# Kernel tuning notes

Hardware: AMD Instinct MI355X
Metric: run time of the kernel (lower is better)

Reference implementation:

```python
import jax, jax.numpy as jnp
import numpy as np

N0, N1, N2 = 60000, 15000, 3750
K, P = 32, 15
R0 = 0.5  # kernel extent at level 0; doubles per level (first_subsampling_dl*deform_radius scaled to unit-cube data)


def kpconv(q_pts, s_pts, neigh_idx, feats, kpoints, W, extent):
    """Rigid KPConv. q_pts [Nq,3], s_pts [Ns,3], neigh_idx [Nq,K] (shadow=Ns),
    feats [Ns,Cin], kpoints [P,3] unit-scale, W [P,Cin,Cout]."""
    s_pts_p = jnp.concatenate([s_pts, jnp.full((1, 3), 1e6, s_pts.dtype)], 0)
    feats_p = jnp.concatenate([feats, jnp.zeros((1, feats.shape[1]), feats.dtype)], 0)
    neigh_pts = s_pts_p[neigh_idx]                       # [Nq,K,3] gather
    neigh_f = feats_p[neigh_idx]                         # [Nq,K,Cin] gather
    diff = neigh_pts - q_pts[:, None, :]                 # [Nq,K,3]
    dist = jnp.sqrt(jnp.sum((diff[:, :, None, :] - kpoints[None, None] * extent) ** 2, -1))
    infl = jnp.maximum(0.0, 1.0 - dist / extent)         # [Nq,K,P] linear influence
    fk = jnp.einsum('nkp,nkc->npc', infl, neigh_f)       # per-kernel-point aggregation
    out = jnp.einsum('npc,pco->no', fk, W)
    return jax.nn.leaky_relu(out, 0.1)


def detection_scores(neighbor, features):
    # verbatim translation of KPFCNN.detection_scores (eval mode)
    n_total = features.shape[0]
    feats = jnp.concatenate([features, jnp.zeros_like(features[:1])], 0)
    neighbor = jnp.concatenate([neighbor, jnp.full_like(neighbor[:1], n_total)], 0)
    feats = feats / (jnp.max(feats) + 1e-6)
    nf = feats[neighbor]                                 # [N+1,K,C]
    nnum = jnp.maximum(jnp.sum(jnp.sum(nf, -1) != 0, -1, keepdims=True), 1)
    mean_f = jnp.sum(nf, 1) / nnum
    local_max_score = jax.nn.softplus(feats - mean_f)
    depth_max = jnp.max(feats, 1, keepdims=True)
    all_scores = local_max_score * (feats / (1e-6 + depth_max))
    scores = jnp.max(all_scores, 1, keepdims=True)
    detected = jnp.max((feats == jnp.max(nf, 1)).astype(feats.dtype), 1, keepdims=True)
    return (scores * detected)[:-1]


def reference(features, points0, points1, points2, neighbors0, neighbors1, neighbors2,
              pools0, pools1, upsamples0, upsamples1, kpoints, W1, W2, W3, W4, W5, Wu1, Wu2):
    # ---- encoder ----
    f = kpconv(points0, points0, neighbors0, features, kpoints, W1, R0)      # simple         [N0,64]
    skip0 = f
    f = kpconv(points1, points0, pools0, f, kpoints, W2, R0)                 # simple_strided [N1,64]
    f = kpconv(points1, points1, neighbors1, f, kpoints, W3, 2 * R0)         # simple         [N1,128]
    skip1 = f
    f = kpconv(points2, points1, pools1, f, kpoints, W4, 2 * R0)             # simple_strided [N2,128]
    f = kpconv(points2, points2, neighbors2, f, kpoints, W5, 4 * R0)         # simple         [N2,256]
    # ---- decoder: nearest_upsample + skip concat + unary ----
    f = jnp.concatenate([f[upsamples1[:, 0]], skip1], 1)                     # [N1,384] (1.5*256)
    f = jax.nn.leaky_relu(f @ Wu1, 0.1)                                      # unary          [N1,128]
    f = jnp.concatenate([f[upsamples0[:, 0]], skip0], 1)                     # [N0,192]
    f = f @ Wu2                                                              # last_unary     [N0,32]
    scores = detection_scores(neighbors0, f)
    fnorm = f / jnp.maximum(jnp.linalg.norm(f, axis=-1, keepdims=True), 1e-12)
    return fnorm, scores


def setup_inputs() -> dict:
    key = jax.random.key(0)
    ks = jax.random.split(key, 20)
    inp = {
        'features': jax.random.normal(ks[0], (N0, 1), jnp.float32),
        'points0': jax.random.uniform(ks[1], (N0, 3), jnp.float32),
        'points1': jax.random.uniform(ks[2], (N1, 3), jnp.float32),
        'points2': jax.random.uniform(ks[3], (N2, 3), jnp.float32),
        'neighbors0': jax.random.randint(ks[4], (N0, K), 0, N0, jnp.int32),
        'neighbors1': jax.random.randint(ks[5], (N1, K), 0, N1, jnp.int32),
        'neighbors2': jax.random.randint(ks[6], (N2, K), 0, N2, jnp.int32),
        'pools0': jax.random.randint(ks[7], (N1, K), 0, N0, jnp.int32),
        'pools1': jax.random.randint(ks[8], (N2, K), 0, N1, jnp.int32),
        'upsamples0': jax.random.randint(ks[9], (N0, 1), 0, N1, jnp.int32),
        'upsamples1': jax.random.randint(ks[10], (N1, 1), 0, N2, jnp.int32),
        'kpoints': jax.random.normal(ks[11], (P, 3), jnp.float32) * 0.5,
    }
    def w(k, shape, fan_in):
        return jax.random.normal(k, shape, jnp.float32) / np.sqrt(fan_in)
    inp['W1'] = w(ks[12], (P, 1, 64), P * 1)
    inp['W2'] = w(ks[13], (P, 64, 64), P * 64)
    inp['W3'] = w(ks[14], (P, 64, 128), P * 64)
    inp['W4'] = w(ks[15], (P, 128, 128), P * 128)
    inp['W5'] = w(ks[16], (P, 128, 256), P * 128)
    inp['Wu1'] = w(ks[17], (384, 128), 384)
    inp['Wu2'] = w(ks[18], (192, 32), 192)
    return inp
```

## Files before the change

### kernel.cpp

```cpp
#include <hip/hip_runtime.h>
#include <math.h>

static const int cN0 = 60000;
static const int cN1 = 15000;
static const int cN2 = 3750;

typedef __bf16 bf16x8 __attribute__((ext_vector_type(8)));
typedef float f32x4 __attribute__((ext_vector_type(4)));

#define GLOAD_LDS16(gsrc, ldst)                                                        \
  __builtin_amdgcn_global_load_lds((const __attribute__((address_space(1))) void*)(gsrc), \
                                   (__attribute__((address_space(3))) void*)(ldst), 16, 0, 0)

__global__ __launch_bounds__(256) void prep_kernel(
    const float* __restrict__ pts0, const float* __restrict__ feat,
    const float* __restrict__ pts1, const float* __restrict__ pts2,
    const float* __restrict__ W2, const float* __restrict__ W3, const float* __restrict__ W4,
    const float* __restrict__ W5, const float* __restrict__ Wu1, const float* __restrict__ Wu2,
    float4* __restrict__ pk0, float4* __restrict__ pk1, float4* __restrict__ pk2,
    __bf16* __restrict__ T2, __bf16* __restrict__ T3, __bf16* __restrict__ T4,
    __bf16* __restrict__ T5, __bf16* __restrict__ Tu1, __bf16* __restrict__ Tu2,
    unsigned* __restrict__ gm) {
  int role = blockIdx.y;
  int tid = blockIdx.x * 256 + threadIdx.x;
  int stride = gridDim.x * 256;
  if (role == 0 && tid == 0) gm[0] = 0u;
  if (role < 3) {
    const float* p = role == 0 ? pts0 : (role == 1 ? pts1 : pts2);
    float4* o = role == 0 ? pk0 : (role == 1 ? pk1 : pk2);
    int n = role == 0 ? cN0 : (role == 1 ? cN1 : cN2);
    for (int i = tid; i < n; i += stride) {
      float4 v;
      v.x = p[(size_t)i * 3 + 0];
      v.y = p[(size_t)i * 3 + 1];
      v.z = p[(size_t)i * 3 + 2];
      v.w = role == 0 ? feat[i] : 0.f;
      o[i] = v;
    }
  } else {
    const float* src;
    __bf16* dst;
    int Kd, Nd;
    switch (role) {
      case 3: src = W2;  dst = T2;  Kd = 960;  Nd = 64;  break;
      case 4: src = W3;  dst = T3;  Kd = 960;  Nd = 128; break;
      case 5: src = W4;  dst = T4;  Kd = 1920; Nd = 128; break;
      case 6: src = W5;  dst = T5;  Kd = 1920; Nd = 256; break;
      case 7: src = Wu1; dst = Tu1; Kd = 384;  Nd = 128; break;
      default: src = Wu2; dst = Tu2; Kd = 192; Nd = 32;  break;
    }
    int total = Kd * Nd;
    for (int e = tid; e < total; e += stride) {
      int n = e / Kd, k = e % Kd;
      dst[e] = (__bf16)src[(size_t)k * Nd + n];
    }
  }
}

__global__ __launch_bounds__(512) void kpconv_l1(
    const float4* __restrict__ pk, const int* __restrict__ neigh,
    const float* __restrict__ kpts, const float* __restrict__ W1,
    __bf16* __restrict__ f0, float extent) {
  const int t = threadIdx.x;
  const int n0b = blockIdx.x * 32;
  __shared__ float s_nb[32][32][4];
  __shared__ float s_fk[32][16];
  __shared__ float s_W[960];
  for (int i = t; i < 960; i += 512) s_W[i] = W1[i];
  #pragma unroll
  for (int i = 0; i < 2; ++i) {
    int e = t + i * 512;
    int pt = e & 31, k = e >> 5;
    int idx = neigh[(size_t)(n0b + pt) * 32 + k];
    *(float4*)&s_nb[k][pt][0] = pk[idx];
  }
  __syncthreads();
  const int lane = t & 63, wave = t >> 6;
  const int g = lane >> 4, p_raw = lane & 15;
  const int p = p_raw < 15 ? p_raw : 0;
  const int pt = wave * 4 + g;
  const int n = n0b + pt;
  const float inv = 1.f / extent;
  float4 q = pk[n];
  const float kx = q.x + kpts[p * 3 + 0] * extent;
  const float ky = q.y + kpts[p * 3 + 1] * extent;
  const float kz = q.z + kpts[p * 3 + 2] * extent;
  float fk = 0.f;
  #pragma unroll 8
  for (int k = 0; k < 32; ++k) {
    f32x4 rec = *(const f32x4*)&s_nb[k][pt][0];
    float dx = rec[0] - kx, dy = rec[1] - ky, dz = rec[2] - kz;
    float d = sqrtf(dx * dx + dy * dy + dz * dz);
    fk += fmaxf(0.f, 1.f - d * inv) * rec[3];
  }
  if (p_raw < 15) s_fk[pt][p_raw] = fk;
  __syncthreads();
  #pragma unroll
  for (int o = 0; o < 4; ++o) {
    int e = o * 512 + t;
    int opt = e >> 6, c = e & 63;
    float acc = 0.f;
    #pragma unroll
    for (int pp = 0; pp < 15; ++pp) acc += s_fk[opt][pp] * s_W[pp * 64 + c];
    acc = acc > 0.f ? acc : 0.1f * acc;
    f0[(size_t)(n0b + opt) * 64 + c] = (__bf16)acc;
  }
}

template <int CIN, int COUT, int BM, bool BDBUF>
__global__ __launch_bounds__(512) void kpconv_fused(
    const float4* __restrict__ qp, const float4* __restrict__ sp,
    const int* __restrict__ neigh, const __bf16* __restrict__ F,
    const float* __restrict__ kpts, const __bf16* __restrict__ BT,
    __bf16* __restrict__ out, int M, float extent) {
  constexpr int KK = 15 * CIN;
  constexpr int KT = KK / 64;
  constexpr int CPRow = CIN / 8;
  constexpr int G = CIN / 64;
  constexpr int GS = 64 / G;
  constexpr int NB = BM / 2;
  constexpr int CPW = CIN / 64;
  constexpr int FBUF = 64 * CIN;
  constexpr int RG = BM / 16;
  constexpr int CG = 8 / RG;
  constexpr int NJ = COUT / (16 * CG);
  constexpr int SMEM_FK = BM * KK * 2;
  constexpr int SMEM = SMEM_FK + 2 * 1280 + BM * 16 + 2 * FBUF * 2;

  __shared__ __align__(16) char smem[SMEM];
  __bf16* s_fk   = (__bf16*)smem;
  __bf16* s_infl = (__bf16*)(smem + SMEM_FK);
  float4* s_q    = (float4*)(smem + SMEM_FK + 2 * 1280);
  __bf16* s_F    = (__bf16*)(smem + SMEM_FK + 2 * 1280 + BM * 16);
  __bf16* s_B    = s_F;

  const int t = threadIdx.x;
  const int w = t >> 6, l = t & 63;
  const int c16 = l & 15, g4 = l >> 4;
  const int m0 = blockIdx.x * BM;
  const int* nb_base = neigh + (size_t)m0 * 32;
  int rlim = (M - m0) * 32 - 1;
  if (rlim > BM * 32 - 1) rlim = BM * 32 - 1;

  const int gb = t / CPRow;
  const int ch = t % CPRow;
  int idxg[NB][G];
  #pragma unroll
  for (int b = 0; b < NB; ++b)
    #pragma unroll
    for (int j = 0; j < G; ++j) {
      int r = b * 64 + gb + j * GS;
      idxg[b][j] = nb_base[r < rlim ? r : rlim];
    }
  const int row_i = (t >> 2) & 63;
  const int pq4 = (t & 3) * 4;
  const int pt_i = row_i >> 5, kk_i = row_i & 31;
  int idxi[NB];
  #pragma unroll
  for (int b = 0; b < NB; ++b) {
    int r = b * 64 + row_i;
    idxi[b] = nb_base[r < rlim ? r : rlim];
  }
  const float inv = 1.f / extent;
  float kpx[4], kpy[4], kpz[4];
  #pragma unroll
  for (int pi = 0; pi < 4; ++pi) {
    int p = pq4 + pi; if (p > 14) p = 14;
    kpx[pi] = kpts[p * 3 + 0] * extent;
    kpy[pi] = kpts[p * 3 + 1] * extent;
    kpz[pi] = kpts[p * 3 + 2] * extent;
  }
  if (t < BM) { int n = m0 + t; s_q[t] = qp[n < M ? n : M - 1]; }

  auto stageF = [&](int buf, const int (&ig)[G]) {
    #pragma unroll
    for (int j = 0; j < G; ++j) {
      int k = (gb + j * GS) & 31;
      const __bf16* src = F + (size_t)ig[j] * CIN + (ch ^ ((k >> 3) & 3)) * 8;
      GLOAD_LDS16(src, s_F + buf * FBUF + (j * 512 + t) * 8);
    }
  };
  auto inflC = [&](const float4& spv, int b, float (&v)[4]) {
    float4 q = s_q[b * 2 + pt_i];
    float sx = spv.x - q.x, sy = spv.y - q.y, sz = spv.z - q.z;
    #pragma unroll
    for (int pi = 0; pi < 4; ++pi) {
      float dx = sx - kpx[pi], dy = sy - kpy[pi], dz = sz - kpz[pi];
      float d = sqrtf(dx * dx + dy * dy + dz * dz);
      v[pi] = fmaxf(0.f, 1.f - d * inv);
    }
  };
  auto inflStore = [&](const float (&v)[4]) {
    if (t < 256) {
      #pragma unroll
      for (int pi = 0; pi < 4; ++pi) {
        int p = pq4 + pi;
        if (p < 15) s_infl[pt_i * 640 + p * 40 + kk_i] = (__bf16)v[pi];
      }
    }
  };
  auto mfmaBatch = [&](int b, int buf) {
    const int pt_loc = w / 4;
    const int cc0 = (w & 3) * CPW;
    const __bf16* Fb = s_F + buf * FBUF + pt_loc * (32 * CIN);
    bf16x8 a = *(const bf16x8*)&s_infl[pt_loc * 640 + c16 * 40 + g4 * 8];
    const int row = b * 2 + pt_loc;
    #pragma unroll
    for (int ci = 0; ci < CPW; ++ci) {
      const int cc = cc0 + ci;
      const int Lc = cc * 2 + (c16 >> 3);
      const int pc = Lc ^ g4;
      bf16x8 bv;
      #pragma unroll
      for (int j = 0; j < 8; ++j)
        bv[j] = Fb[(g4 * 8 + j) * CIN + pc * 8 + (c16 & 7)];
      f32x4 acc = __builtin_amdgcn_mfma_f32_16x16x32_bf16(a, bv, (f32x4){0.f, 0.f, 0.f, 0.f}, 0, 0, 0);
      #pragma unroll
      for (int r = 0; r < 4; ++r) {
        int p = g4 * 4 + r;
        if (p < 15) {
          int Lf = p * CPRow + Lc;
          int phys = (Lf & ~7) | ((Lf & 7) ^ (row & 7));
          s_fk[(size_t)row * KK + phys * 8 + (c16 & 7)] = (__bf16)acc[r];
        }
      }
    }
  };

  asm volatile("s_waitcnt lgkmcnt(0)" ::: "memory");
  __builtin_amdgcn_s_barrier();
  __builtin_amdgcn_sched_barrier(0);

  float4 spc, spn;
  {
    stageF(0, idxg[0]);
    float4 sp0 = sp[idxi[0]];
    spc = sp[idxi[1 < NB ? 1 : 0]];
    float v0[4];
    inflC(sp0, 0, v0);
    inflStore(v0);
  }
  __builtin_amdgcn_sched_barrier(0);
  #pragma unroll
  for (int b = 0; b < NB; ++b) {
    if (b + 1 < NB) stageF((b + 1) & 1, idxg[b + 1]);
    if (b + 2 < NB) spn = sp[idxi[b + 2]];
    float vn[4];
    if (b + 1 < NB) inflC(spc, b + 1, vn);
    if (b == NB - 1)      { asm volatile("s_waitcnt vmcnt(0)" ::: "memory"); }
    else if (b == NB - 2) { if (G == 1) asm volatile("s_waitcnt vmcnt(1)" ::: "memory");
                            else        asm volatile("s_waitcnt vmcnt(2)" ::: "memory"); }
    else                  { if (G == 1) asm volatile("s_waitcnt vmcnt(2)" ::: "memory");
                            else        asm volatile("s_waitcnt vmcnt(3)" ::: "memory"); }
    asm volatile("s_waitcnt lgkmcnt(0)" ::: "memory");
    __builtin_amdgcn_s_barrier();
    __builtin_amdgcn_sched_barrier(0);
    mfmaBatch(b, b & 1);
    asm volatile("s_waitcnt lgkmcnt(0)" ::: "memory");
    __builtin_amdgcn_s_barrier();
    __builtin_amdgcn_sched_barrier(0);
    if (b + 1 < NB) { inflStore(vn); spc = spn; }
  }
  __syncthreads();

  const int wr = w / CG, wc = w % CG;
  f32x4 acc[NJ];
  #pragma unroll
  for (int j = 0; j < NJ; ++j) acc[j] = (f32x4){0.f, 0.f, 0.f, 0.f};
  auto stageB = [&](int buf, int kt) {
    #pragma unroll
    for (int rnd = 0; rnd < COUT / 64; ++rnd) {
      int slot = rnd * 512 + t;
      int row = slot >> 3, bch = slot & 7;
      GLOAD_LDS16(BT + (size_t)row * KK + kt * 64 + (bch ^ (row & 7)) * 8,
                  s_B + buf * (COUT * 64) + slot * 8);
    }
  };
  const __bf16* fkrow = s_fk + (size_t)(wr * 16 + c16) * KK;
  auto computeTile = [&](int kt, int buf) {
    bf16x8 af[2];
    #pragma unroll
    for (int s = 0; s < 2; ++s)
      af[s] = *(const bf16x8*)&fkrow[(kt * 8 + ((s * 4 + g4) ^ (c16 & 7))) * 8];
    const __bf16* Bb = s_B + buf * (COUT * 64);
    #pragma unroll
    for (int j = 0; j < NJ; ++j) {
      int n = wc * (16 * NJ) + j * 16 + c16;
      #pragma unroll
      for (int s = 0; s < 2; ++s) {
        bf16x8 bf = *(const bf16x8*)&Bb[n * 64 + ((s * 4 + g4) ^ (n & 7)) * 8];
        acc[j] = __builtin_amdgcn_mfma_f32_16x16x32_bf16(af[s], bf, acc[j], 0, 0, 0);
      }
    }
  };
  if (BDBUF) {
    stageB(0, 0);
    __syncthreads();
    for (int kt = 0; kt < KT; ++kt) {
      if (kt + 1 < KT) stageB((kt + 1) & 1, kt + 1);
      computeTile(kt, kt & 1);
      __syncthreads();
    }
  } else {
    for (int kt = 0; kt < KT; ++kt) {
      stageB(0, kt);
      __syncthreads();
      computeTile(kt, 0);
      __syncthreads();
    }
  }
  #pragma unroll
  for (int j = 0; j < NJ; ++j)
    #pragma unroll
    for (int r = 0; r < 4; ++r) {
      int row = m0 + wr * 16 + g4 * 4 + r;
      int col = wc * (16 * NJ) + j * 16 + c16;
      if (row < M) {
        float v = acc[j][r];
        v = v > 0.f ? v : 0.1f * v;
        out[(size_t)row * COUT + col] = (__bf16)v;
      }
    }
}

template <bool LEAKY, bool GATHER>
__global__ __launch_bounds__(256, 2) void gemm_mfma(
    const __bf16* __restrict__ A1, const __bf16* __restrict__ A2,
    const int* __restrict__ gidx, const int K1,
    const __bf16* __restrict__ BT, __bf16* __restrict__ Cout,
    const int M, const int N, const int KK) {
  __shared__ __bf16 sA[2][4096];
  __shared__ __bf16 sB[2][4096];
  const int t = threadIdx.x;
  const int lane = t & 63, wave = t >> 6;
  const int wr = wave >> 1, wc = wave & 1;
  const int m0 = blockIdx.y * 64, n0 = blockIdx.x * 64;
  const int K2 = KK - K1;

  const __bf16* a1row[2];
  const __bf16* a2row[2];
  const __bf16* brow_[2];
  int csrc[2], wbase[2];
  #pragma unroll
  for (int r = 0; r < 2; ++r) {
    int slot = r * 256 + wave * 64 + lane;
    int row = slot >> 3;
    csrc[r] = ((slot & 7) ^ (row & 7)) * 8;
    wbase[r] = (r * 256 + wave * 64) * 8;
    int gm = m0 + row; if (gm > M - 1) gm = M - 1;
    if (GATHER) {
      a1row[r] = A1 + (size_t)gidx[gm] * K1;
      a2row[r] = A2 + (size_t)gm * (size_t)K2;
    } else {
      a1row[r] = A1 + (size_t)gm * (size_t)KK;
    }
    int gn = n0 + row; if (gn > N - 1) gn = N - 1;
    brow_[r] = BT + (size_t)gn * (size_t)KK;
  }

  int offA[2][2], offB[2][2];
  #pragma unroll
  for (int i = 0; i < 2; ++i)
    #pragma unroll
    for (int s = 0; s < 2; ++s) {
      int ra = wr * 32 + i * 16 + (lane & 15);
      int rb = wc * 32 + i * 16 + (lane & 15);
      int chn = s * 4 + (lane >> 4);
      offA[i][s] = ra * 64 + (chn ^ (ra & 7)) * 8;
      offB[i][s] = rb * 64 + (chn ^ (rb & 7)) * 8;
    }

  f32x4 acc[2][2];
  #pragma unroll
  for (int i = 0; i < 2; ++i)
    #pragma unroll
    for (int j = 0; j < 2; ++j) acc[i][j] = (f32x4){0.f, 0.f, 0.f, 0.f};

  auto stage = [&](int buf, int k0) {
    #pragma unroll
    for (int r = 0; r < 2; ++r) {
      int kg = k0 + csrc[r];
      const __bf16* asrc;
      if (GATHER) asrc = (kg < K1) ? (a1row[r] + kg) : (a2row[r] + (kg - K1));
      else        asrc = a1row[r] + kg;
      GLOAD_LDS16(asrc, &sA[buf][wbase[r]]);
      GLOAD_LDS16(brow_[r] + kg, &sB[buf][wbase[r]]);
    }
  };

  stage(0, 0);
  __syncthreads();
  const int nk = KK >> 6;
  int cur = 0;
  for (int kt = 0; kt < nk; ++kt) {
    if (kt + 1 < nk) stage(cur ^ 1, (kt + 1) << 6);
    #pragma unroll
    for (int s = 0; s < 2; ++s) {
      bf16x8 a0 = *(const bf16x8*)&sA[cur][offA[0][s]];
      bf16x8 a1 = *(const bf16x8*)&sA[cur][offA[1][s]];
      bf16x8 b0 = *(const bf16x8*)&sB[cur][offB[0][s]];
      bf16x8 b1 = *(const bf16x8*)&sB[cur][offB[1][s]];
      acc[0][0] = __builtin_amdgcn_mfma_f32_16x16x32_bf16(a0, b0, acc[0][0], 0, 0, 0);
      acc[0][1] = __builtin_amdgcn_mfma_f32_16x16x32_bf16(a0, b1, acc[0][1], 0, 0, 0);
      acc[1][0] = __builtin_amdgcn_mfma_f32_16x16x32_bf16(a1, b0, acc[1][0], 0, 0, 0);
      acc[1][1] = __builtin_amdgcn_mfma_f32_16x16x32_bf16(a1, b1, acc[1][1], 0, 0, 0);
    }
    __syncthreads();
    cur ^= 1;
  }

  #pragma unroll
  for (int i = 0; i < 2; ++i)
    #pragma unroll
    for (int j = 0; j < 2; ++j)
      #pragma unroll
      for (int g = 0; g < 4; ++g) {
        int row = m0 + wr * 32 + i * 16 + (lane >> 4) * 4 + g;
        int col = n0 + wc * 32 + j * 16 + (lane & 15);
        if (row < M && col < N) {
          float v = acc[i][j][g];
          if (LEAKY) v = v > 0.f ? v : 0.1f * v;
          Cout[(size_t)row * N + col] = (__bf16)v;
        }
      }
}

__global__ __launch_bounds__(256) void d2_kernel(
    const __bf16* __restrict__ f5b, const __bf16* __restrict__ f0b,
    const int* __restrict__ up0, const __bf16* __restrict__ BT,
    float* __restrict__ f6, int M, unsigned* __restrict__ gmax) {
  __shared__ __bf16 sA[128 * 192];
  __shared__ __bf16 sB[32 * 192];
  __shared__ int s_g[128];
  __shared__ float s_max[4];
  const int t = threadIdx.x;
  const int m0 = blockIdx.x * 128;
  if (t < 128) { int m = m0 + t; s_g[t] = up0[m < M ? m : M - 1]; }
  __syncthreads();
  #pragma unroll
  for (int rnd = 0; rnd < 3; ++rnd) {
    int slot = rnd * 256 + t;
    int row = slot / 24, chd = slot % 24;
    int chs = (chd & ~7) | ((chd & 7) ^ (row & 7));
    GLOAD_LDS16(BT + (size_t)row * 192 + chs * 8, sB + slot * 8);
  }
  #pragma unroll
  for (int rnd = 0; rnd < 12; ++rnd) {
    int slot = rnd * 256 + t;
    int row = slot / 24, chd = slot % 24;
    int chs = (chd & ~7) | ((chd & 7) ^ (row & 7));
    int m = m0 + row; if (m > M - 1) m = M - 1;
    const __bf16* src = (chs < 16) ? (f5b + (size_t)s_g[row] * 128 + chs * 8)
                                   : (f0b + (size_t)m * 64 + (chs - 16) * 8);
    GLOAD_LDS16(src, sA + slot * 8);
  }
  __syncthreads();
  const int w = t >> 6, lane = t & 63;
  const int c16 = lane & 15, g4 = lane >> 4;
  f32x4 acc[2][2];
  #pragma unroll
  for (int i = 0; i < 2; ++i)
    #pragma unroll
    for (int j = 0; j < 2; ++j) acc[i][j] = (f32x4){0.f, 0.f, 0.f, 0.f};
  #pragma unroll
  for (int ks = 0; ks < 6; ++ks) {
    bf16x8 a[2], b[2];
    #pragma unroll
    for (int i = 0; i < 2; ++i) {
      int row = w * 32 + i * 16 + c16;
      int chunk = ks * 4 + g4;
      int phys = (chunk & ~7) | ((chunk & 7) ^ (row & 7));
      a[i] = *(const bf16x8*)&sA[(row * 24 + phys) * 8];
    }
    #pragma unroll
    for (int j = 0; j < 2; ++j) {
      int n = j * 16 + c16;
      int chunk = ks * 4 + g4;
      int phys = (chunk & ~7) | ((chunk & 7) ^ (n & 7));
      b[j] = *(const bf16x8*)&sB[(n * 24 + phys) * 8];
    }
    #pragma unroll
    for (int i = 0; i < 2; ++i)
      #pragma unroll
      for (int j = 0; j < 2; ++j)
        acc[i][j] = __builtin_amdgcn_mfma_f32_16x16x32_bf16(a[i], b[j], acc[i][j], 0, 0, 0);
  }
  float lmax = 0.f;
  #pragma unroll
  for (int i = 0; i < 2; ++i)
    #pragma unroll
    for (int j = 0; j < 2; ++j)
      #pragma unroll
      for (int g = 0; g < 4; ++g) {
        int row = m0 + w * 32 + i * 16 + g4 * 4 + g;
        int col = j * 16 + c16;
        if (row < M) {
          float v = acc[i][j][g];
          lmax = fmaxf(lmax, v);
          f6[(size_t)row * 32 + col] = v;
        }
      }
  #pragma unroll
  for (int s = 32; s >= 1; s >>= 1) lmax = fmaxf(lmax, __shfl_xor(lmax, s, 64));
  if (lane == 0) s_max[w] = lmax;
  __syncthreads();
  if (t == 0) {
    float mm = fmaxf(fmaxf(s_max[0], s_max[1]), fmaxf(s_max[2], s_max[3]));
    atomicMax(gmax, __float_as_uint(mm));
  }
}

__global__ __launch_bounds__(512) void detect_kernel(
    const float* __restrict__ f6, const int* __restrict__ neigh,
    const float* __restrict__ gm_ptr, float* __restrict__ out_fnorm,
    float* __restrict__ out_scores, int N) {
  int n = blockIdx.x * 16 + (threadIdx.x >> 5);
  int c = threadIdx.x & 31;
  if (n >= N) return;
  float denom = gm_ptr[0] + 1e-6f;
  float fown = f6[(size_t)n * 32 + c];
  int idx_l = neigh[(size_t)n * 32 + c];
  float colsum = 0.f, colmax = -1e30f;
  for (int k = 0; k < 32; ++k) {
    int idx = __shfl(idx_l, k, 32);
    float v = f6[(size_t)idx * 32 + c];
    colsum += v;
    colmax = fmaxf(colmax, v);
  }
  float fs = fown / denom;
  float mean = (colsum / denom) * (1.f / 32.f);
  float x = fs - mean;
  float lms = fmaxf(x, 0.f) + log1pf(expf(-fabsf(x)));
  float dm = fs;
  #pragma unroll
  for (int s = 16; s >= 1; s >>= 1) dm = fmaxf(dm, __shfl_xor(dm, s, 32));
  float as = lms * fs / (1e-6f + dm);
  float sc = as;
  #pragma unroll
  for (int s = 16; s >= 1; s >>= 1) sc = fmaxf(sc, __shfl_xor(sc, s, 32));
  float det = (fown == colmax) ? 1.f : 0.f;
  #pragma unroll
  for (int s = 16; s >= 1; s >>= 1) det = fmaxf(det, __shfl_xor(det, s, 32));
  float nn2 = fown * fown;
  #pragma unroll
  for (int s = 16; s >= 1; s >>= 1) nn2 += __shfl_xor(nn2, s, 32);
  float inv_nrm = 1.f / fmaxf(sqrtf(nn2), 1e-12f);
  out_fnorm[(size_t)n * 32 + c] = fown * inv_nrm;
  if (c == 0) out_scores[n] = sc * det;
}

extern "C" void kernel_launch(void* const* d_in, const int* in_sizes, int n_in,
                              void* d_out, int out_size, void* d_ws, size_t ws_size,
                              hipStream_t stream) {
  const float* features  = (const float*)d_in[0];
  const float* points0   = (const float*)d_in[1];
  const float* points1   = (const float*)d_in[2];
  const float* points2   = (const float*)d_in[3];
  const int* neighbors0  = (const int*)d_in[4];
  const int* neighbors1  = (const int*)d_in[5];
  const int* neighbors2  = (const int*)d_in[6];
  const int* pools0      = (const int*)d_in[7];
  const int* pools1      = (const int*)d_in[8];
  const int* upsamples0  = (const int*)d_in[9];
  const int* upsamples1  = (const int*)d_in[10];
  const float* kpoints   = (const float*)d_in[11];
  const float* W1  = (const float*)d_in[12];
  const float* W2  = (const float*)d_in[13];
  const float* W3  = (const float*)d_in[14];
  const float* W4  = (const float*)d_in[15];
  const float* W5  = (const float*)d_in[16];
  const float* Wu1 = (const float*)d_in[17];
  const float* Wu2 = (const float*)d_in[18];

  const float R0 = 0.5f;

  char* wp = (char*)d_ws;
  auto alloc = [&](size_t bytes) {
    char* r = wp;
    wp += (bytes + 255) & ~(size_t)255;
    return r;
  };
  __bf16* f0b  = (__bf16*)alloc((size_t)cN0 * 64 * 2);
  __bf16* f1b  = (__bf16*)alloc((size_t)cN1 * 64 * 2);
  __bf16* f2b  = (__bf16*)alloc((size_t)cN1 * 128 * 2);
  __bf16* f3b  = (__bf16*)alloc((size_t)cN2 * 128 * 2);
  __bf16* f4b  = (__bf16*)alloc((size_t)cN2 * 256 * 2);
  __bf16* f5b  = (__bf16*)alloc((size_t)cN1 * 128 * 2);
  float*  f6   = (float*)alloc((size_t)cN0 * 32 * 4);
  __bf16* WT2  = (__bf16*)alloc(960 * 64 * 2);
  __bf16* WT3  = (__bf16*)alloc(960 * 128 * 2);
  __bf16* WT4  = (__bf16*)alloc(1920 * 128 * 2);
  __bf16* WT5  = (__bf16*)alloc(1920 * 256 * 2);
  __bf16* WTu1 = (__bf16*)alloc(384 * 128 * 2);
  __bf16* WTu2 = (__bf16*)alloc(192 * 32 * 2);
  unsigned* gm = (unsigned*)alloc(256);
  float4* pk0  = (float4*)alloc((size_t)cN0 * 16);
  float4* pk1  = (float4*)alloc((size_t)cN1 * 16);
  float4* pk2  = (float4*)alloc((size_t)cN2 * 16);

  prep_kernel<<<dim3(240, 9), 256, 0, stream>>>(
      points0, features, points1, points2, W2, W3, W4, W5, Wu1, Wu2,
      pk0, pk1, pk2, WT2, WT3, WT4, WT5, WTu1, WTu2, gm);
  kpconv_l1<<<cN0 / 32, 512, 0, stream>>>(pk0, neighbors0, kpoints, W1, f0b, R0);

  kpconv_fused<64, 64, 32, true><<<(cN1 + 31) / 32, 512, 0, stream>>>(
      pk1, pk0, pools0, f0b, kpoints, WT2, f1b, cN1, R0);
  kpconv_fused<64, 128, 32, false><<<(cN1 + 31) / 32, 512, 0, stream>>>(
      pk1, pk1, neighbors1, f1b, kpoints, WT3, f2b, cN1, 2.f * R0);
  kpconv_fused<128, 128, 16, true><<<(cN2 + 15) / 16, 512, 0, stream>>>(
      pk2, pk1, pools1, f2b, kpoints, WT4, f3b, cN2, 2.f * R0);
  kpconv_fused<128, 256, 16, false><<<(cN2 + 15) / 16, 512, 0, stream>>>(
      pk2, pk2, neighbors2, f3b, kpoints, WT5, f4b, cN2, 4.f * R0);

  gemm_mfma<true, true><<<dim3(2, 235), 256, 0, stream>>>(
      f4b, f2b, upsamples1, 256, WTu1, f5b, cN1, 128, 384);
  d2_kernel<<<(cN0 + 127) / 128, 256, 0, stream>>>(
      f5b, f0b, upsamples0, WTu2, f6, cN0, gm);

  float* out_fnorm = (float*)d_out;
  float* out_scores = out_fnorm + (size_t)cN0 * 32;
  detect_kernel<<<(cN0 + 15) / 16, 512, 0, stream>>>(f6, neighbors0, (const float*)gm,
                                                     out_fnorm, out_scores, cN0);
}
```

Baseline: 203.0 us.

## Triple-buffer gather stage to drop one barrier per batch in level-2 kpconv

Adds a template flag that triple-buffers the gathered neighbor features and influence weights in LDS for the two CIN=128 kpconv launches. With three buffers the loop needs only one barrier per batch instead of two, and the influence weights are stored before the wait, so gathers overlap the MFMA work more. This costs extra LDS per block, which may lower occupancy. The detect kernel's neighbor loop is also unrolled by four.

```diff
diff --git a/kernel.cpp b/kernel.cpp
--- a/kernel.cpp
+++ b/kernel.cpp
@@ -107,7 +107,7 @@
   }
 }
 
-template <int CIN, int COUT, int BM, bool BDBUF>
+template <int CIN, int COUT, int BM, bool BDBUF, bool SB>
 __global__ __launch_bounds__(512) void kpconv_fused(
     const float4* __restrict__ qp, const float4* __restrict__ sp,
     const int* __restrict__ neigh, const __bf16* __restrict__ F,
@@ -121,17 +121,19 @@
   constexpr int NB = BM / 2;
   constexpr int CPW = CIN / 64;
   constexpr int FBUF = 64 * CIN;
+  constexpr int NFB = SB ? 3 : 2;
+  constexpr int NIB = SB ? 3 : 1;
   constexpr int RG = BM / 16;
   constexpr int CG = 8 / RG;
   constexpr int NJ = COUT / (16 * CG);
   constexpr int SMEM_FK = BM * KK * 2;
-  constexpr int SMEM = SMEM_FK + 2 * 1280 + BM * 16 + 2 * FBUF * 2;
+  constexpr int SMEM = SMEM_FK + NIB * 2560 + BM * 16 + NFB * FBUF * 2;
 
   __shared__ __align__(16) char smem[SMEM];
   __bf16* s_fk   = (__bf16*)smem;
   __bf16* s_infl = (__bf16*)(smem + SMEM_FK);
-  float4* s_q    = (float4*)(smem + SMEM_FK + 2 * 1280);
-  __bf16* s_F    = (__bf16*)(smem + SMEM_FK + 2 * 1280 + BM * 16);
+  float4* s_q    = (float4*)(smem + SMEM_FK + NIB * 2560);
+  __bf16* s_F    = (__bf16*)(smem + SMEM_FK + NIB * 2560 + BM * 16);
   __bf16* s_B    = s_F;
 
   const int t = threadIdx.x;
@@ -190,20 +192,20 @@
       v[pi] = fmaxf(0.f, 1.f - d * inv);
     }
   };
-  auto inflStore = [&](const float (&v)[4]) {
+  auto inflStore = [&](const float (&v)[4], int ibuf) {
     if (t < 256) {
       #pragma unroll
       for (int pi = 0; pi < 4; ++pi) {
         int p = pq4 + pi;
-        if (p < 15) s_infl[pt_i * 640 + p * 40 + kk_i] = (__bf16)v[pi];
-      }
-    }
-  };
-  auto mfmaBatch = [&](int b, int buf) {
+        if (p < 15) s_infl[ibuf * 1280 + pt_i * 640 + p * 40 + kk_i] = (__bf16)v[pi];
+      }
+    }
+  };
+  auto mfmaBatch = [&](int b, int fbuf, int ibuf) {
     const int pt_loc = w / 4;
     const int cc0 = (w & 3) * CPW;
-    const __bf16* Fb = s_F + buf * FBUF + pt_loc * (32 * CIN);
-    bf16x8 a = *(const bf16x8*)&s_infl[pt_loc * 640 + c16 * 40 + g4 * 8];
+    const __bf16* Fb = s_F + fbuf * FBUF + pt_loc * (32 * CIN);
+    bf16x8 a = *(const bf16x8*)&s_infl[ibuf * 1280 + pt_loc * 640 + c16 * 40 + g4 * 8];
     const int row = b * 2 + pt_loc;
     #pragma unroll
     for (int ci = 0; ci < CPW; ++ci) {
@@ -232,36 +234,74 @@
   __builtin_amdgcn_sched_barrier(0);
 
   float4 spc, spn;
-  {
+  if (SB) {
     stageF(0, idxg[0]);
     float4 sp0 = sp[idxi[0]];
     spc = sp[idxi[1 < NB ? 1 : 0]];
     float v0[4];
     inflC(sp0, 0, v0);
-    inflStore(v0);
-  }
-  __builtin_amdgcn_sched_barrier(0);
-  #pragma unroll
-  for (int b = 0; b < NB; ++b) {
-    if (b + 1 < NB) stageF((b + 1) & 1, idxg[b + 1]);
-    if (b + 2 < NB) spn = sp[idxi[b + 2]];
-    float vn[4];
-    if (b + 1 < NB) inflC(spc, b + 1, vn);
-    if (b == NB - 1)      { asm volatile("s_waitcnt vmcnt(0)" ::: "memory"); }
-    else if (b == NB - 2) { if (G == 1) asm volatile("s_waitcnt vmcnt(1)" ::: "memory");
-                            else        asm volatile("s_waitcnt vmcnt(2)" ::: "memory"); }
-    else                  { if (G == 1) asm volatile("s_waitcnt vmcnt(2)" ::: "memory");
-                            else        asm volatile("s_waitcnt vmcnt(3)" ::: "memory"); }
+    inflStore(v0, 0);
+    __builtin_amdgcn_sched_barrier(0);
     asm volatile("s_waitcnt lgkmcnt(0)" ::: "memory");
     __builtin_amdgcn_s_barrier();
     __builtin_amdgcn_sched_barrier(0);
-    mfmaBatch(b, b & 1);
-    asm volatile("s_waitcnt lgkmcnt(0)" ::: "memory");
-    __builtin_amdgcn_s_barrier();
+    #pragma unroll
+    for (int b = 0; b < NB; ++b) {
+      if (b + 1 < NB) stageF((b + 1) % 3, idxg[b + 1]);
+      if (b + 2 < NB) spn = sp[idxi[b + 2]];
+      if (b + 1 < NB) {
+        float vn[4];
+        inflC(spc, b + 1, vn);
+        inflStore(vn, (b + 1) % 3);
+        if (b + 2 < NB) spc = spn;
+      }
+      __builtin_amdgcn_sched_barrier(0);
+      if (b + 1 < NB) {
+        if (b + 2 < NB) { if (G == 1) asm volatile("s_waitcnt vmcnt(2)" ::: "memory");
+                          else        asm volatile("s_waitcnt vmcnt(3)" ::: "memory"); }
+        else            { if (G == 1) asm volatile("s_waitcnt vmcnt(1)" ::: "memory");
+                          else        asm volatile("s_waitcnt vmcnt(2)" ::: "memory"); }
+      } else {
+        asm volatile("s_waitcnt vmcnt(0)" ::: "memory");
+      }
+      asm volatile("s_waitcnt lgkmcnt(0)" ::: "memory");
+      __builtin_amdgcn_s_barrier();
+      __builtin_amdgcn_sched_barrier(0);
+      mfmaBatch(b, b % 3, b % 3);
+    }
+    __syncthreads();
+  } else {
+    {
+      stageF(0, idxg[0]);
+      float4 sp0 = sp[idxi[0]];
+      spc = sp[idxi[1 < NB ? 1 : 0]];
+      float v0[4];
+      inflC(sp0, 0, v0);
+      inflStore(v0, 0);
+    }
     __builtin_amdgcn_sched_barrier(0);
-    if (b + 1 < NB) { inflStore(vn); spc = spn; }
-  }
-  __syncthreads();
+    #pragma unroll
+    for (int b = 0; b < NB; ++b) {
+      if (b + 1 < NB) stageF((b + 1) & 1, idxg[b + 1]);
+      if (b + 2 < NB) spn = sp[idxi[b + 2]];
+      float vn[4];
+      if (b + 1 < NB) inflC(spc, b + 1, vn);
+      if (b == NB - 1)      { asm volatile("s_waitcnt vmcnt(0)" ::: "memory"); }
+      else if (b == NB - 2) { if (G == 1) asm volatile("s_waitcnt vmcnt(1)" ::: "memory");
+                              else        asm volatile("s_waitcnt vmcnt(2)" ::: "memory"); }
+      else                  { if (G == 1) asm volatile("s_waitcnt vmcnt(2)" ::: "memory");
+                              else        asm volatile("s_waitcnt vmcnt(3)" ::: "memory"); }
+      asm volatile("s_waitcnt lgkmcnt(0)" ::: "memory");
+      __builtin_amdgcn_s_barrier();
+      __builtin_amdgcn_sched_barrier(0);
+      mfmaBatch(b, b & 1, 0);
+      asm volatile("s_waitcnt lgkmcnt(0)" ::: "memory");
+      __builtin_amdgcn_s_barrier();
+      __builtin_amdgcn_sched_barrier(0);
+      if (b + 1 < NB) { inflStore(vn, 0); spc = spn; }
+    }
+    __syncthreads();
+  }
 
   const int wr = w / CG, wc = w % CG;
   f32x4 acc[NJ];
@@ -521,6 +561,7 @@
   float fown = f6[(size_t)n * 32 + c];
   int idx_l = neigh[(size_t)n * 32 + c];
   float colsum = 0.f, colmax = -1e30f;
+  #pragma unroll 4
   for (int k = 0; k < 32; ++k) {
     int idx = __shfl(idx_l, k, 32);
     float v = f6[(size_t)idx * 32 + c];
@@ -603,13 +644,13 @@
       pk0, pk1, pk2, WT2, WT3, WT4, WT5, WTu1, WTu2, gm);
   kpconv_l1<<<cN0 / 32, 512, 0, stream>>>(pk0, neighbors0, kpoints, W1, f0b, R0);
 
-  kpconv_fused<64, 64, 32, true><<<(cN1 + 31) / 32, 512, 0, stream>>>(
+  kpconv_fused<64, 64, 32, true, false><<<(cN1 + 31) / 32, 512, 0, stream>>>(
       pk1, pk0, pools0, f0b, kpoints, WT2, f1b, cN1, R0);
-  kpconv_fused<64, 128, 32, false><<<(cN1 + 31) / 32, 512, 0, stream>>>(
+  kpconv_fused<64, 128, 32, false, false><<<(cN1 + 31) / 32, 512, 0, stream>>>(
       pk1, pk1, neighbors1, f1b, kpoints, WT3, f2b, cN1, 2.f * R0);
-  kpconv_fused<128, 128, 16, true><<<(cN2 + 15) / 16, 512, 0, stream>>>(
+  kpconv_fused<128, 128, 16, true, true><<<(cN2 + 15) / 16, 512, 0, stream>>>(
       pk2, pk1, pools1, f2b, kpoints, WT4, f3b, cN2, 2.f * R0);
-  kpconv_fused<128, 256, 16, false><<<(cN2 + 15) / 16, 512, 0, stream>>>(
+  kpconv_fused<128, 256, 16, false, true><<<(cN2 + 15) / 16, 512, 0, stream>>>(
       pk2, pk2, neighbors2, f3b, kpoints, WT5, f4b, cN2, 4.f * R0);
 
   gemm_mfma<true, true><<<dim3(2, 235), 256, 0, stream>>>(
```

After: 207.0 us. Within noise of the previous version (+2.0%).
